# Kernel optimization log

Hardware: AMD Instinct MI355X
Metric: run time of the kernel (lower is better)

## Reference

```python
import jax, jax.numpy as jnp
import numpy as np

CUTOFF = 5.0
NUM_RADIAL = 6
HIDDEN = 128
N_NODES = 100000
N_EDGES = 800000
MAX_Z = 95
P = 6  # envelope_exponent(5) + 1, per PyG Envelope


def _envelope(x):
    # PyG DimeNet Envelope: (1/x + a*x^(p-1) + b*x^p + c*x^(p+1)) * (x < 1)
    a = -(P + 1) * (P + 2) / 2.0   # -28
    b = P * (P + 2)                # 48
    c = -P * (P + 1) / 2.0         # -21
    xp0 = x ** (P - 1)
    xp1 = xp0 * x
    xp2 = xp1 * x
    return (1.0 / x + a * xp0 + b * xp1 + c * xp2) * (x < 1.0)


def setup_inputs():
    key = jax.random.key(0)
    ks = jax.random.split(key, 8)
    z = jax.random.randint(ks[0], (N_NODES,), 0, MAX_Z, dtype=jnp.int32)
    pos = jax.random.normal(ks[1], (N_NODES, 3), dtype=jnp.float32)
    ei = jax.random.randint(ks[2], (2, N_EDGES), 0, N_NODES, dtype=jnp.int32)
    i, j = ei[0], ei[1]
    j = jnp.where(j == i, (j + 1) % N_NODES, j)  # radius_graph emits no self-loops (avoids d=0)
    edge_index = jnp.stack([i, j])
    # BesselBasisLayer learnable frequencies: pi * n
    freq = np.pi * jnp.arange(1, NUM_RADIAL + 1, dtype=jnp.float32)
    s3 = float(np.sqrt(3.0))
    emb_table = jax.random.uniform(ks[3], (MAX_Z, HIDDEN), jnp.float32, -s3, s3)
    W_rbf = jax.random.normal(ks[4], (NUM_RADIAL, HIDDEN), jnp.float32) * (1.0 / np.sqrt(NUM_RADIAL))
    b_rbf = jnp.zeros((HIDDEN,), jnp.float32)
    W_lin = jax.random.normal(ks[5], (3 * HIDDEN, HIDDEN), jnp.float32) * (1.0 / np.sqrt(3 * HIDDEN))
    b_lin = jnp.zeros((HIDDEN,), jnp.float32)
    return {"z": z, "pos": pos, "edge_index": edge_index, "freq": freq,
            "emb_table": emb_table, "W_rbf": W_rbf, "b_rbf": b_rbf,
            "W_lin": W_lin, "b_lin": b_lin}


def reference(z, pos, edge_index, freq, emb_table, W_rbf, b_rbf, W_lin, b_lin):
    n = z.shape[0]
    i, j = edge_index[0], edge_index[1]
    # per-edge distance  [E]
    d = jnp.sqrt(jnp.sum((pos[i] - pos[j]) ** 2, axis=-1))
    # Bessel RBF  [E, num_radial]
    x = d[:, None] / CUTOFF
    rbf = _envelope(x) * jnp.sin(freq * x)
    # DimeNet EmbeddingBlock (act = SiLU/swish)
    h_rbf = jax.nn.silu(rbf @ W_rbf + b_rbf)            # [E, H]
    xz = emb_table[z]                                    # [N, H]
    e_emb = jax.nn.silu(
        jnp.concatenate([xz[i], xz[j], h_rbf], axis=-1) @ W_lin + b_lin
    )                                                    # [E, H]
    # scatter_mean over target node j -> [N, H]
    sums = jax.ops.segment_sum(e_emb, j, num_segments=n)
    cnt = jax.ops.segment_sum(jnp.ones_like(d), j, num_segments=n)
    v_emb = sums / jnp.maximum(cnt, 1.0)[:, None]
    return v_emb  # pool=None -> node-level embeddings
```

## Files before the change

### kernel.cpp

```cpp
#include <hip/hip_runtime.h>
#include <hip/hip_bf16.h>
#include <math.h>

#define HID 128
#define NRAD 6
#define TABN 4096
#define CUTOFF_INV 0.2f
#define MZ 95

typedef unsigned int uint32;

__global__ void build1(const float* __restrict__ emb, const float* __restrict__ W_lin,
                       const float* __restrict__ freq, const float* __restrict__ W_rbf,
                       const float* __restrict__ b_rbf, const float* __restrict__ b_lin,
                       __hip_bfloat16* __restrict__ Tb, float* __restrict__ ftab,
                       const int* __restrict__ ej, int* __restrict__ cnt,
                       int* __restrict__ rank, int MAXZ, int E) {
    __shared__ float sh[HID];
    int h   = threadIdx.x;
    int bid = blockIdx.x;
    int nT  = 2 * MAXZ;
    int nF  = TABN + 1;
    if (bid < nT) {
        int zz = bid >> 1, s = bid & 1;
        sh[h] = emb[zz * HID + h];
        __syncthreads();
        const float* W = W_lin + (size_t)s * HID * HID;
        float acc = (s == 0) ? b_lin[h] : 0.f;
#pragma unroll 8
        for (int k = 0; k < HID; ++k) acc = fmaf(sh[k], W[k * HID + h], acc);
        Tb[(size_t)(s * MAXZ + zz) * HID + h] = __float2bfloat16(acc);
    } else if (bid < nT + nF) {
        int t = bid - nT;
        float rbf[NRAD];
        if (t == 0) {
#pragma unroll
            for (int k = 0; k < NRAD; ++k) rbf[k] = freq[k];
        } else if (t >= TABN) {
#pragma unroll
            for (int k = 0; k < NRAD; ++k) rbf[k] = 0.f;
        } else {
            float x  = (float)t / (float)TABN;
            float x2 = x * x, x5 = x2 * x2 * x;
            float env = 1.f / x + x5 * (-28.f + x * (48.f + x * (-21.f)));
#pragma unroll
            for (int k = 0; k < NRAD; ++k) rbf[k] = env * sinf(freq[k] * x);
        }
        float pre = b_rbf[h];
#pragma unroll
        for (int k = 0; k < NRAD; ++k) pre = fmaf(rbf[k], W_rbf[k * HID + h], pre);
        sh[h] = pre / (1.f + __expf(-pre));
        __syncthreads();
        const float* W3 = W_lin + (size_t)2 * HID * HID;
        float acc = 0.f;
#pragma unroll 8
        for (int k = 0; k < HID; ++k) acc = fmaf(sh[k], W3[k * HID + h], acc);
        ftab[(size_t)t * HID + h] = acc;
    } else {
        int e = (bid - nT - nF) * HID + h;
        if (e < E) rank[e] = atomicAdd(&cnt[ej[e]], 1);
    }
}

__global__ void scan1(const int* __restrict__ cnt, int* __restrict__ offs,
                      int* __restrict__ bsum) {
    int t = threadIdx.x;
    size_t base = (size_t)blockIdx.x * 1024 + t * 4;
    int4 v = *(const int4*)(cnt + base);
    int s0 = v.x, s1 = s0 + v.y, s2 = s1 + v.z, s3 = s2 + v.w;
    int lane = t & 63, wv = t >> 6;
    int incl = s3;
#pragma unroll
    for (int off = 1; off < 64; off <<= 1) {
        int u = __shfl_up(incl, off, 64);
        if (lane >= off) incl += u;
    }
    __shared__ int ws[4];
    if (lane == 63) ws[wv] = incl;
    __syncthreads();
    int wbase = 0;
    for (int w = 0; w < wv; ++w) wbase += ws[w];
    int ex = wbase + incl - s3;
    int4 o;
    o.x = ex; o.y = ex + s0; o.z = ex + s1; o.w = ex + s2;
    *(int4*)(offs + base) = o;
    if (t == 255) bsum[blockIdx.x] = wbase + incl;
}

__global__ void scan2(int* __restrict__ bsum, int NB) {
    int t = threadIdx.x;
    int v = (t < NB) ? bsum[t] : 0;
    int lane = t & 63, wv = t >> 6;
    int incl = v;
#pragma unroll
    for (int off = 1; off < 64; off <<= 1) {
        int u = __shfl_up(incl, off, 64);
        if (lane >= off) incl += u;
    }
    __shared__ int ws[4];
    if (lane == 63) ws[wv] = incl;
    __syncthreads();
    int wbase = 0;
    for (int w = 0; w < wv; ++w) wbase += ws[w];
    if (t < NB) bsum[t] = wbase + incl - v;
}

__global__ void scan3(int* __restrict__ offs, const int* __restrict__ bsum) {
    size_t base = (size_t)blockIdx.x * 1024 + threadIdx.x * 4;
    int add = bsum[blockIdx.x];
    int4 o = *(int4*)(offs + base);
    o.x += add; o.y += add; o.z += add; o.w += add;
    *(int4*)(offs + base) = o;
}

__global__ void scatter_k(const int* __restrict__ ei, const float* __restrict__ pos,
                          const int* __restrict__ z, const int* __restrict__ offs,
                          const int* __restrict__ rank, int* __restrict__ payload, int E) {
    int e = blockIdx.x * 256 + threadIdx.x;
    if (e >= E) return;
    int i = ei[e];
    int j = ei[E + e];
    float dx = pos[3 * i]     - pos[3 * j];
    float dy = pos[3 * i + 1] - pos[3 * j + 1];
    float dz = pos[3 * i + 2] - pos[3 * j + 2];
    float d  = sqrtf(dx * dx + dy * dy + dz * dz);
    float u  = fminf(d * CUTOFF_INV, 1.0f) * (float)TABN;
    int   ti = (int)(u + 0.5f);
    if (ti > TABN) ti = TABN;
    int pl = ti | (z[i] << 13) | (z[j] << 20);
    payload[offs[j] + rank[e]] = pl;
}

__launch_bounds__(1024)
__global__ void gather_k(const int* __restrict__ offs, const int* __restrict__ payload,
                         const uint32* __restrict__ Tb32, const float* __restrict__ ftab,
                         float* __restrict__ out, int N) {
    __shared__ uint32 sT[2 * MZ * (HID / 2)];
    int tid = threadIdx.x;
    for (int k = tid; k < 2 * MZ * (HID / 2); k += 1024) sT[k] = Tb32[k];
    __syncthreads();

    int lane = tid & 63, wv = tid >> 6;
    int h2   = lane * 2;
    const uint32* sT2 = sT + MZ * (HID / 2);
    const float*  ft  = ftab + h2;
    int nCh = (N + 15) >> 4;

    for (int ch = blockIdx.x; ch < nCh; ch += gridDim.x) {
        int n = (ch << 4) + wv;
        if (n >= N) continue;
        int beg = offs[n];
        int end = offs[n + 1];

        float a0 = 0.f, a1 = 0.f;
        for (int base = beg; base < end; base += 64) {
            int rem = end - base;
            int cb  = rem < 64 ? rem : 64;
            int plv = payload[base + (lane < cb ? lane : cb - 1)];
            for (int k = 0; k < cb; ++k) {
                int pl = __builtin_amdgcn_readlane(plv, k);
                int ti = pl & 0x1FFF;
                int zi = (pl >> 13) & 0x7F;
                int zj = (pl >> 20) & 0x7F;
                float2 f  = *(const float2*)(ft + (size_t)ti * HID);
                uint32 u1 = sT[zi * (HID / 2) + lane];
                uint32 u2 = sT2[zj * (HID / 2) + lane];
                float p0 = __uint_as_float(u1 << 16)         + __uint_as_float(u2 << 16)         + f.x;
                float p1 = __uint_as_float(u1 & 0xFFFF0000u) + __uint_as_float(u2 & 0xFFFF0000u) + f.y;
                a0 = fmaf(p0, __builtin_amdgcn_rcpf(1.f + __expf(-p0)), a0);
                a1 = fmaf(p1, __builtin_amdgcn_rcpf(1.f + __expf(-p1)), a1);
            }
        }
        float s = (end > beg) ? 1.0f / (float)(end - beg) : 0.0f;
        float2 o; o.x = a0 * s; o.y = a1 * s;
        *(float2*)(out + (size_t)n * HID + h2) = o;
    }
}

extern "C" void kernel_launch(void* const* d_in, const int* in_sizes, int n_in,
                              void* d_out, int out_size, void* d_ws, size_t ws_size,
                              hipStream_t stream) {
    const int*   z     = (const int*)d_in[0];
    const float* pos   = (const float*)d_in[1];
    const int*   ei    = (const int*)d_in[2];
    const float* freq  = (const float*)d_in[3];
    const float* emb   = (const float*)d_in[4];
    const float* W_rbf = (const float*)d_in[5];
    const float* b_rbf = (const float*)d_in[6];
    const float* W_lin = (const float*)d_in[7];
    const float* b_lin = (const float*)d_in[8];

    int N    = in_sizes[0];
    int E    = in_sizes[2] / 2;
    int MAXZ = in_sizes[4] / HID;
    float* out = (float*)d_out;

    int N_pad = ((N + 1024) / 1024) * 1024;
    int NB    = N_pad / 1024;

    char* ws = (char*)d_ws;
    size_t off = 0;
    auto alloc = [&](size_t bytes) { char* p = ws + off; off = (off + bytes + 255) & ~(size_t)255; return p; };
    int*   cnt     = (int*)alloc((size_t)N_pad * 4);
    int*   offs    = (int*)alloc((size_t)N_pad * 4);
    int*   bsum    = (int*)alloc((size_t)NB * 4);
    int*   rank    = (int*)alloc((size_t)E * 4);
    __hip_bfloat16* Tb = (__hip_bfloat16*)alloc((size_t)2 * MAXZ * HID * 2);
    float* ftab    = (float*)alloc((size_t)(TABN + 1) * HID * 4);
    int*   payload = (int*)alloc((size_t)E * 4);

    hipMemsetAsync(cnt, 0, (size_t)N_pad * 4, stream);

    int nBuild = 2 * MAXZ + (TABN + 1) + (E + HID - 1) / HID;
    build1<<<nBuild, HID, 0, stream>>>(emb, W_lin, freq, W_rbf, b_rbf, b_lin,
                                       Tb, ftab, ei + E, cnt, rank, MAXZ, E);
    scan1<<<NB, 256, 0, stream>>>(cnt, offs, bsum);
    scan2<<<1, 256, 0, stream>>>(bsum, NB);
    scan3<<<NB, 256, 0, stream>>>(offs, bsum);
    scatter_k<<<(E + 255) / 256, 256, 0, stream>>>(ei, pos, z, offs, rank, payload, E);
    gather_k<<<512, 1024, 0, stream>>>(offs, payload, (const uint32*)Tb, ftab, out, N);
}
```

Measured before the change: 214.1 us.

## Replace CSR scan with fixed-slot per-node buckets plus overflow fixup

Result: faster. 190.9 us (-10.9%).

```diff
diff --git a/kernel.cpp b/kernel.cpp
--- a/kernel.cpp
+++ b/kernel.cpp
@@ -7,15 +7,20 @@
 #define TABN 4096
 #define CUTOFF_INV 0.2f
 #define MZ 95
+#define PAD 32
+#define OVF_CAP 65536
 
 typedef unsigned int uint32;
 
 __global__ void build1(const float* __restrict__ emb, const float* __restrict__ W_lin,
                        const float* __restrict__ freq, const float* __restrict__ W_rbf,
                        const float* __restrict__ b_rbf, const float* __restrict__ b_lin,
+                       const int* __restrict__ ei, const float* __restrict__ pos,
+                       const int* __restrict__ z,
                        __hip_bfloat16* __restrict__ Tb, float* __restrict__ ftab,
-                       const int* __restrict__ ej, int* __restrict__ cnt,
-                       int* __restrict__ rank, int MAXZ, int E) {
+                       int* __restrict__ cnt, int* __restrict__ payload,
+                       int* __restrict__ ovfcnt, int2* __restrict__ ovfbuf,
+                       int MAXZ, int E) {
     __shared__ float sh[HID];
     int h   = threadIdx.x;
     int bid = blockIdx.x;
@@ -58,81 +63,30 @@
         ftab[(size_t)t * HID + h] = acc;
     } else {
         int e = (bid - nT - nF) * HID + h;
-        if (e < E) rank[e] = atomicAdd(&cnt[ej[e]], 1);
+        if (e < E) {
+            int i = ei[e];
+            int j = ei[E + e];
+            float dx = pos[3 * i]     - pos[3 * j];
+            float dy = pos[3 * i + 1] - pos[3 * j + 1];
+            float dz = pos[3 * i + 2] - pos[3 * j + 2];
+            float d  = sqrtf(dx * dx + dy * dy + dz * dz);
+            float u  = fminf(d * CUTOFF_INV, 1.0f) * (float)TABN;
+            int   ti = (int)(u + 0.5f);
+            if (ti > TABN) ti = TABN;
+            int pl = ti | (z[i] << 13) | (z[j] << 20);
+            int r  = atomicAdd(&cnt[j], 1);
+            if (r < PAD) {
+                payload[j * PAD + r] = pl;
+            } else {
+                int o = atomicAdd(ovfcnt, 1);
+                if (o < OVF_CAP) ovfbuf[o] = make_int2(j, pl);
+            }
+        }
     }
 }
 
-__global__ void scan1(const int* __restrict__ cnt, int* __restrict__ offs,
-                      int* __restrict__ bsum) {
-    int t = threadIdx.x;
-    size_t base = (size_t)blockIdx.x * 1024 + t * 4;
-    int4 v = *(const int4*)(cnt + base);
-    int s0 = v.x, s1 = s0 + v.y, s2 = s1 + v.z, s3 = s2 + v.w;
-    int lane = t & 63, wv = t >> 6;
-    int incl = s3;
-#pragma unroll
-    for (int off = 1; off < 64; off <<= 1) {
-        int u = __shfl_up(incl, off, 64);
-        if (lane >= off) incl += u;
-    }
-    __shared__ int ws[4];
-    if (lane == 63) ws[wv] = incl;
-    __syncthreads();
-    int wbase = 0;
-    for (int w = 0; w < wv; ++w) wbase += ws[w];
-    int ex = wbase + incl - s3;
-    int4 o;
-    o.x = ex; o.y = ex + s0; o.z = ex + s1; o.w = ex + s2;
-    *(int4*)(offs + base) = o;
-    if (t == 255) bsum[blockIdx.x] = wbase + incl;
-}
-
-__global__ void scan2(int* __restrict__ bsum, int NB) {
-    int t = threadIdx.x;
-    int v = (t < NB) ? bsum[t] : 0;
-    int lane = t & 63, wv = t >> 6;
-    int incl = v;
-#pragma unroll
-    for (int off = 1; off < 64; off <<= 1) {
-        int u = __shfl_up(incl, off, 64);
-        if (lane >= off) incl += u;
-    }
-    __shared__ int ws[4];
-    if (lane == 63) ws[wv] = incl;
-    __syncthreads();
-    int wbase = 0;
-    for (int w = 0; w < wv; ++w) wbase += ws[w];
-    if (t < NB) bsum[t] = wbase + incl - v;
-}
-
-__global__ void scan3(int* __restrict__ offs, const int* __restrict__ bsum) {
-    size_t base = (size_t)blockIdx.x * 1024 + threadIdx.x * 4;
-    int add = bsum[blockIdx.x];
-    int4 o = *(int4*)(offs + base);
-    o.x += add; o.y += add; o.z += add; o.w += add;
-    *(int4*)(offs + base) = o;
-}
-
-__global__ void scatter_k(const int* __restrict__ ei, const float* __restrict__ pos,
-                          const int* __restrict__ z, const int* __restrict__ offs,
-                          const int* __restrict__ rank, int* __restrict__ payload, int E) {
-    int e = blockIdx.x * 256 + threadIdx.x;
-    if (e >= E) return;
-    int i = ei[e];
-    int j = ei[E + e];
-    float dx = pos[3 * i]     - pos[3 * j];
-    float dy = pos[3 * i + 1] - pos[3 * j + 1];
-    float dz = pos[3 * i + 2] - pos[3 * j + 2];
-    float d  = sqrtf(dx * dx + dy * dy + dz * dz);
-    float u  = fminf(d * CUTOFF_INV, 1.0f) * (float)TABN;
-    int   ti = (int)(u + 0.5f);
-    if (ti > TABN) ti = TABN;
-    int pl = ti | (z[i] << 13) | (z[j] << 20);
-    payload[offs[j] + rank[e]] = pl;
-}
-
 __launch_bounds__(1024)
-__global__ void gather_k(const int* __restrict__ offs, const int* __restrict__ payload,
+__global__ void gather_k(const int* __restrict__ cnt, const int* __restrict__ payload,
                          const uint32* __restrict__ Tb32, const float* __restrict__ ftab,
                          float* __restrict__ out, int N) {
     __shared__ uint32 sT[2 * MZ * (HID / 2)];
@@ -149,31 +103,53 @@
     for (int ch = blockIdx.x; ch < nCh; ch += gridDim.x) {
         int n = (ch << 4) + wv;
         if (n >= N) continue;
-        int beg = offs[n];
-        int end = offs[n + 1];
+        int deg = cnt[n];
+        int cb  = deg < PAD ? deg : PAD;
+        int plv = payload[n * PAD + (lane & (PAD - 1))];
 
         float a0 = 0.f, a1 = 0.f;
-        for (int base = beg; base < end; base += 64) {
-            int rem = end - base;
-            int cb  = rem < 64 ? rem : 64;
-            int plv = payload[base + (lane < cb ? lane : cb - 1)];
-            for (int k = 0; k < cb; ++k) {
-                int pl = __builtin_amdgcn_readlane(plv, k);
-                int ti = pl & 0x1FFF;
-                int zi = (pl >> 13) & 0x7F;
-                int zj = (pl >> 20) & 0x7F;
-                float2 f  = *(const float2*)(ft + (size_t)ti * HID);
-                uint32 u1 = sT[zi * (HID / 2) + lane];
-                uint32 u2 = sT2[zj * (HID / 2) + lane];
-                float p0 = __uint_as_float(u1 << 16)         + __uint_as_float(u2 << 16)         + f.x;
-                float p1 = __uint_as_float(u1 & 0xFFFF0000u) + __uint_as_float(u2 & 0xFFFF0000u) + f.y;
-                a0 = fmaf(p0, __builtin_amdgcn_rcpf(1.f + __expf(-p0)), a0);
-                a1 = fmaf(p1, __builtin_amdgcn_rcpf(1.f + __expf(-p1)), a1);
-            }
+        for (int k = 0; k < cb; ++k) {
+            int pl = __builtin_amdgcn_readlane(plv, k);
+            int ti = pl & 0x1FFF;
+            int zi = (pl >> 13) & 0x7F;
+            int zj = (pl >> 20) & 0x7F;
+            float2 f  = *(const float2*)(ft + (size_t)ti * HID);
+            uint32 u1 = sT[zi * (HID / 2) + lane];
+            uint32 u2 = sT2[zj * (HID / 2) + lane];
+            float p0 = __uint_as_float(u1 << 16)         + __uint_as_float(u2 << 16)         + f.x;
+            float p1 = __uint_as_float(u1 & 0xFFFF0000u) + __uint_as_float(u2 & 0xFFFF0000u) + f.y;
+            a0 = fmaf(p0, __builtin_amdgcn_rcpf(1.f + __expf(-p0)), a0);
+            a1 = fmaf(p1, __builtin_amdgcn_rcpf(1.f + __expf(-p1)), a1);
         }
-        float s = (end > beg) ? 1.0f / (float)(end - beg) : 0.0f;
+        float s = (deg > 0) ? 1.0f / (float)deg : 0.0f;
         float2 o; o.x = a0 * s; o.y = a1 * s;
         *(float2*)(out + (size_t)n * HID + h2) = o;
+    }
+}
+
+__global__ void fixup_k(const int* __restrict__ ovfcnt, const int2* __restrict__ ovfbuf,
+                        const int* __restrict__ cnt, const uint32* __restrict__ Tb32,
+                        const float* __restrict__ ftab, float* __restrict__ out, int MAXZ) {
+    int nov = *ovfcnt;
+    if (nov > OVF_CAP) nov = OVF_CAP;
+    int total = nov * 64;
+    int stride = gridDim.x * blockDim.x;
+    const uint32* T2b = Tb32 + MAXZ * (HID / 2);
+    for (int u = blockIdx.x * blockDim.x + threadIdx.x; u < total; u += stride) {
+        int ent = u >> 6, lane = u & 63;
+        int2 v = ovfbuf[ent];
+        int j  = v.x, pl = v.y;
+        int ti = pl & 0x1FFF;
+        int zi = (pl >> 13) & 0x7F;
+        int zj = (pl >> 20) & 0x7F;
+        float2 f  = *(const float2*)(ftab + (size_t)ti * HID + lane * 2);
+        uint32 u1 = Tb32[zi * (HID / 2) + lane];
+        uint32 u2 = T2b[zj * (HID / 2) + lane];
+        float p0 = __uint_as_float(u1 << 16)         + __uint_as_float(u2 << 16)         + f.x;
+        float p1 = __uint_as_float(u1 & 0xFFFF0000u) + __uint_as_float(u2 & 0xFFFF0000u) + f.y;
+        float s  = 1.0f / (float)max(cnt[j], 1);
+        atomicAdd(&out[(size_t)j * HID + lane * 2],     p0 * __builtin_amdgcn_rcpf(1.f + __expf(-p0)) * s);
+        atomicAdd(&out[(size_t)j * HID + lane * 2 + 1], p1 * __builtin_amdgcn_rcpf(1.f + __expf(-p1)) * s);
     }
 }
 
@@ -196,27 +172,23 @@
     float* out = (float*)d_out;
 
     int N_pad = ((N + 1024) / 1024) * 1024;
-    int NB    = N_pad / 1024;
 
     char* ws = (char*)d_ws;
     size_t off = 0;
     auto alloc = [&](size_t bytes) { char* p = ws + off; off = (off + bytes + 255) & ~(size_t)255; return p; };
     int*   cnt     = (int*)alloc((size_t)N_pad * 4);
-    int*   offs    = (int*)alloc((size_t)N_pad * 4);
-    int*   bsum    = (int*)alloc((size_t)NB * 4);
-    int*   rank    = (int*)alloc((size_t)E * 4);
+    int*   ovfcnt  = (int*)alloc(256);
     __hip_bfloat16* Tb = (__hip_bfloat16*)alloc((size_t)2 * MAXZ * HID * 2);
     float* ftab    = (float*)alloc((size_t)(TABN + 1) * HID * 4);
-    int*   payload = (int*)alloc((size_t)E * 4);
+    int*   payload = (int*)alloc((size_t)N_pad * PAD * 4);
+    int2*  ovfbuf  = (int2*)alloc((size_t)OVF_CAP * 8);
 
-    hipMemsetAsync(cnt, 0, (size_t)N_pad * 4, stream);
+    hipMemsetAsync(cnt, 0, (size_t)N_pad * 4 + 256, stream);
 
     int nBuild = 2 * MAXZ + (TABN + 1) + (E + HID - 1) / HID;
     build1<<<nBuild, HID, 0, stream>>>(emb, W_lin, freq, W_rbf, b_rbf, b_lin,
-                                       Tb, ftab, ei + E, cnt, rank, MAXZ, E);
-    scan1<<<NB, 256, 0, stream>>>(cnt, offs, bsum);
-    scan2<<<1, 256, 0, stream>>>(bsum, NB);
-    scan3<<<NB, 256, 0, stream>>>(offs, bsum);
-    scatter_k<<<(E + 255) / 256, 256, 0, stream>>>(ei, pos, z, offs, rank, payload, E);
-    gather_k<<<512, 1024, 0, stream>>>(offs, payload, (const uint32*)Tb, ftab, out, N);
+                                       ei, pos, z, Tb, ftab, cnt, payload,
+                                       ovfcnt, ovfbuf, MAXZ, E);
+    gather_k<<<512, 1024, 0, stream>>>(cnt, payload, (const uint32*)Tb, ftab, out, N);
+    fixup_k<<<128, 256, 0, stream>>>(ovfcnt, ovfbuf, cnt, (const uint32*)Tb, ftab, out, MAXZ);
 }
```
